# Performance work log

Hardware: AMD Instinct MI355X
Metric: run time of the kernel (lower is better)

The kernel has to match this reference:

```python
import jax, jax.numpy as jnp
import numpy as np
from jax import lax

B, N, T, NX = 4, 512, 24, 8
H = 64
PRED_LEN, NY = 12, 1
E_RAND = 8192
EPS = 1e-5


def setup_inputs() -> dict:
    key = jax.random.key(0)
    ks = jax.random.split(key, 24)
    sc = lambda k, shape: (jax.random.normal(k, shape, jnp.float32) * 0.05)
    x = jax.random.normal(ks[0], (B, N, T, NX), jnp.float32)
    er = jax.random.randint(ks[1], (2, E_RAND), 0, N, dtype=jnp.int32)
    loops = jnp.stack([jnp.arange(N, dtype=jnp.int32), jnp.arange(N, dtype=jnp.int32)])
    edge_index = jnp.concatenate([er, loops], axis=1)  # [2, 8704]
    return {
        'x': x,
        'edge_index': edge_index,
        'W_fc': sc(ks[2], (NX, H)), 'b_fc': jnp.zeros((H,), jnp.float32),
        'W1': sc(ks[3], (H, H)), 'a_l1': sc(ks[4], (H,)), 'a_r1': sc(ks[5], (H,)), 'bias1': jnp.zeros((H,), jnp.float32),
        'W2': sc(ks[6], (H, H)), 'a_l2': sc(ks[7], (H,)), 'a_r2': sc(ks[8], (H,)), 'bias2': jnp.zeros((H,), jnp.float32),
        'W_ih': sc(ks[9], (4 * H, H)), 'W_hh': sc(ks[10], (4 * H, H)),
        'b_ih': jnp.zeros((4 * H,), jnp.float32), 'b_hh': jnp.zeros((4 * H,), jnp.float32),
        'g_l': jnp.ones((H,), jnp.float32), 'b_l': jnp.zeros((H,), jnp.float32),
        'g_g': jnp.ones((H,), jnp.float32), 'b_g': jnp.zeros((H,), jnp.float32),
        'W_d': sc(ks[11], (H, PRED_LEN * NY)), 'b_d': jnp.zeros((PRED_LEN * NY,), jnp.float32),
    }


def _layer_norm(x, g, b):
    mu = jnp.mean(x, axis=-1, keepdims=True)
    var = jnp.mean(jnp.square(x - mu), axis=-1, keepdims=True)
    return (x - mu) * lax.rsqrt(var + EPS) * g + b


def _gat(x, W, a_l, a_r, bias, mask):
    # x: [B,N,T,F] -> operate in [B,T,N,H] layout (torch transpose(1,2))
    h = jnp.einsum('bntf,fh->btnh', x, W)          # [B,T,N,H]
    el = jnp.einsum('btnh,h->btn', h, a_l)          # attn_l
    er = jnp.einsum('btnh,h->btn', h, a_r)          # attn_r
    e = el[..., :, None] + er[..., None, :]         # [B,T,N,N]
    e = jax.nn.leaky_relu(e, negative_slope=0.2)
    e = jnp.where(mask, e, -jnp.inf)
    alpha = jax.nn.softmax(e, axis=-1)
    out = jnp.einsum('btmn,btnh->bmth', alpha, h) + bias  # back to [B,N,T,H]
    return jax.nn.gelu(out, approximate=False)


def _lstm(xseq, W_ih, W_hh, b_ih, b_hh):
    # xseq: [M, T, H] -> outputs [M, T, H]; PyTorch gate order i,f,g,o
    M = xseq.shape[0]
    Hh = W_hh.shape[1]
    b = b_ih + b_hh
    def step(carry, xt):
        hprev, cprev = carry
        gates = xt @ W_ih.T + hprev @ W_hh.T + b
        i, f, g, o = jnp.split(gates, 4, axis=-1)
        c = jax.nn.sigmoid(f) * cprev + jax.nn.sigmoid(i) * jnp.tanh(g)
        h = jax.nn.sigmoid(o) * jnp.tanh(c)
        return (h, c), h
    init = (jnp.zeros((M, Hh), xseq.dtype), jnp.zeros((M, Hh), xseq.dtype))
    _, hs = lax.scan(step, init, xseq.transpose(1, 0, 2))  # [T,M,H]
    return hs.transpose(1, 0, 2)


def reference(x, edge_index, W_fc, b_fc, W1, a_l1, a_r1, bias1, W2, a_l2, a_r2, bias2,
              W_ih, W_hh, b_ih, b_hh, g_l, b_l, g_g, b_g, W_d, b_d):
    Bb, Nn, Tt, _ = x.shape
    mask = jnp.zeros((Nn, Nn), bool).at[edge_index[0], edge_index[1]].set(True)
    x_h = jnp.einsum('bntf,fh->bnth', x, W_fc) + b_fc          # fc
    g1 = _gat(x_h, W1, a_l1, a_r1, bias1, mask)                # conv1
    g2 = _gat(g1, W2, a_l2, a_r2, bias2, mask)                 # conv2
    l = _lstm(x_h.reshape(Bb * Nn, Tt, -1), W_ih, W_hh, b_ih, b_hh).reshape(Bb, Nn, Tt, -1)
    h = _layer_norm(g2, g_g, b_g) + _layer_norm(l, g_l, b_l)
    last = h[:, :, -1, :]                                       # [B,N,H]
    out = last @ W_d + b_d                                      # [B,N,pred_len*ny]
    return out.reshape(Bb, Nn, PRED_LEN, NY)
```

## Files before the change

### kernel.cpp

```cpp
#include <hip/hip_runtime.h>
#include <hip/hip_bf16.h>
#include <math.h>

#define BB 4
#define NN 512
#define TT 24
#define NXF 8
#define HH 64
#define PRED 12
#define MM (BB*NN)

typedef __attribute__((ext_vector_type(8))) short short8;
typedef __attribute__((ext_vector_type(4))) float f32x4;

#define WS_HBUF    0
#define WS_H2      131072
#define WS_G2      262144
#define WS_EL      393216
#define WS_ER      395264
#define WS_EL2     397312
#define WS_ER2     399360
#define WS_WCOMB   401408
#define WS_BCOMB   403456
#define WS_WHHFRAG 403712

__device__ inline float sigm(float x){ return 1.f/(1.f+__expf(-x)); }
__device__ inline float tanh_fast(float x){ float e=__expf(2.f*x); return 1.f - 2.f/(e+1.f); }
__device__ inline float gelu_exact(float x){ return 0.5f*x*(1.f+erff(x*0.70710678118654752440f)); }
__device__ inline unsigned short f2bu(float f){
    unsigned b=__float_as_uint(f);
    return (unsigned short)((b + 0x7FFFu + ((b>>16)&1u))>>16);
}
__device__ inline float bu2f(unsigned short u){ return __uint_as_float(((unsigned)u)<<16); }

__device__ inline void split8(const float* f, short8& hi, short8& lo){
    #pragma unroll
    for (int j = 0; j < 8; ++j){
        unsigned short h = f2bu(f[j]);
        hi[j] = (short)h;
        lo[j] = (short)f2bu(f[j] - bu2f(h));
    }
}

__global__ __launch_bounds__(256,2) void gat1pre_kernel(
    const float* __restrict__ x, const float* __restrict__ Wfc, const float* __restrict__ bfc,
    const float* __restrict__ W1, const float* __restrict__ al1, const float* __restrict__ ar1,
    const float* __restrict__ Wih, const float* __restrict__ Whh,
    const float* __restrict__ bih, const float* __restrict__ bhh,
    float* __restrict__ Hbuf, float* __restrict__ el, float* __restrict__ er,
    float* __restrict__ wcombG, float* __restrict__ bcombG,
    unsigned short* __restrict__ whhfrag)
{
    __shared__ float sw1[HH*HH];
    __shared__ float swfc[NXF*HH];
    __shared__ float sb[HH], sal[HH], sar[HH];
    __shared__ float sxh[4][68];
    __shared__ float sx[4][NXF];
    const int t = threadIdx.x;

    if (blockIdx.x >= 512){
        const int f = blockIdx.x - 512;
        const int ng = t;
        float accf = 0.f, accb = 0.f;
        const float* wr = Wih + ng*64;
        #pragma unroll
        for (int k = 0; k < 64; ++k){
            float wv = wr[k];
            accf += Wfc[f*64 + k] * wv;
            accb += bfc[k] * wv;
        }
        wcombG[f*256 + ng] = accf;
        if (f == 0) bcombG[ng] = accb + bih[ng] + bhh[ng];
        #pragma unroll
        for (int u = 0; u < 8; ++u){
            int o = f*2048 + u*256 + t;
            int F  = o >> 9;
            int ln = (o >> 3) & 63;
            int j  = o & 7;
            int w_ = F >> 3, tt = (F >> 1) & 3, ks = F & 1;
            int q = ln >> 4, c = ln & 15;
            int ngx = (w_ + 4*tt)*16 + c;
            whhfrag[o] = f2bu(Whh[ngx*64 + ks*32 + q*8 + j]);
        }
        return;
    }

    const int r = t >> 6, h = t & 63;
    #pragma unroll
    for (int i = 0; i < 16; ++i) sw1[t + 256*i] = W1[t + 256*i];
    swfc[t] = Wfc[t];
    swfc[t+256] = Wfc[t+256];
    if (t < 64) sb[t] = bfc[t];
    else if (t < 128) sal[t-64] = al1[t-64];
    else if (t < 192) sar[t-128] = ar1[t-128];
    if (t < 32){
        int rr = t >> 3, f = t & 7;
        sx[rr][f] = x[(size_t)(blockIdx.x*4 + rr)*(TT*NXF) + (TT-1)*NXF + f];
    }
    __syncthreads();
    float xh = sb[h];
    #pragma unroll
    for (int f = 0; f < NXF; ++f) xh += sx[r][f]*swfc[f*HH + h];
    sxh[r][h] = xh;
    __syncthreads();
    float acc = 0.f;
    const float4* xr = (const float4*)&sxh[r][0];
    #pragma unroll
    for (int k4 = 0; k4 < 16; ++k4){
        float4 xv = xr[k4];
        acc += xv.x*sw1[(4*k4+0)*HH+h] + xv.y*sw1[(4*k4+1)*HH+h]
             + xv.z*sw1[(4*k4+2)*HH+h] + xv.w*sw1[(4*k4+3)*HH+h];
    }
    const int m = blockIdx.x*4 + r;
    Hbuf[(size_t)m*HH + h] = acc;
    float v1 = acc*sal[h], v2 = acc*sar[h];
    #pragma unroll
    for (int o = 32; o; o >>= 1){ v1 += __shfl_xor(v1,o); v2 += __shfl_xor(v2,o); }
    if (h == 0){ el[m] = v1; er[m] = v2; }
}

__global__ __launch_bounds__(256,2) void attn_fuse_kernel(
    const float* __restrict__ Hbuf, const float* __restrict__ el_in, const float* __restrict__ er_in,
    const int* __restrict__ ei, int E,
    const float* __restrict__ bias1,
    const float* __restrict__ W2, const float* __restrict__ al2, const float* __restrict__ ar2,
    float* __restrict__ H2, float* __restrict__ el2, float* __restrict__ er2)
{
    __shared__ unsigned smask[16][16];
    __shared__ float er_s[NN];
    __shared__ float alpha[16][516];
    __shared__ __align__(16) float uSpace[64*70];
    __shared__ float xh2[16][68];
    __shared__ float sal[HH], sar[HH];

    const int t = threadIdx.x;
    const int b = blockIdx.x >> 5;
    const int m0 = (blockIdx.x & 31) * 16;
    const int l = t & 63, w = t >> 6;
    const int quad = l >> 4, c16 = l & 15;
    float (*HT)[70] = (float(*)[70])uSpace;

    if (t < 64) sal[t] = al2[t]; else if (t < 128) sar[t-64] = ar2[t-64];
    ((unsigned*)smask)[t] = 0;
    er_s[t] = er_in[b*NN + t];
    er_s[t+256] = er_in[b*NN + t + 256];
    __syncthreads();
    for (int e = t; e < E; e += 256){
        int s = ei[e];
        unsigned rl = (unsigned)(s - m0);
        if (rl < 16u){
            int d = ei[E + e];
            atomicOr(&smask[rl][d>>5], 1u << (d & 31));
        }
    }
    const float* Hbase = Hbuf + (size_t)b*NN*HH;
    const int nn = t >> 2, cc = t & 3;
    float4 r0,r1,r2,r3;
    {
        const float4* src = (const float4*)(Hbase + (size_t)nn*HH + cc*16);
        r0 = src[0]; r1 = src[1]; r2 = src[2]; r3 = src[3];
    }
    __syncthreads();
    for (int q = 0; q < 4; ++q){
        const int i = w*4 + q;
        const float elv = el_in[b*NN + m0 + i];
        float e8[8]; unsigned mk = 0; float mx = -1e30f;
        #pragma unroll
        for (int j = 0; j < 8; ++j){
            int n = l + 64*j;
            float ev = elv + er_s[n];
            ev = ev >= 0.f ? ev : 0.2f*ev;
            unsigned mb = (smask[i][(l>>5) + 2*j] >> (l & 31)) & 1u;
            e8[j] = ev;
            if (mb){ mk |= (1u<<j); mx = fmaxf(mx, ev); }
        }
        #pragma unroll
        for (int o = 32; o; o >>= 1) mx = fmaxf(mx, __shfl_xor(mx, o));
        float s = 0.f;
        #pragma unroll
        for (int j = 0; j < 8; ++j){
            float p = ((mk>>j) & 1u) ? __expf(e8[j]-mx) : 0.f;
            e8[j] = p; s += p;
        }
        #pragma unroll
        for (int o = 32; o; o >>= 1) s += __shfl_xor(s, o);
        const float inv = 1.f/s;
        #pragma unroll
        for (int j = 0; j < 8; ++j) alpha[i][l + 64*j] = e8[j]*inv;
    }
    __syncthreads();

    f32x4 acc = {0.f,0.f,0.f,0.f};
    for (int tile = 0; tile < 8; ++tile){
        {
            float v[16] = {r0.x,r0.y,r0.z,r0.w, r1.x,r1.y,r1.z,r1.w,
                           r2.x,r2.y,r2.z,r2.w, r3.x,r3.y,r3.z,r3.w};
            #pragma unroll
            for (int jj = 0; jj < 16; ++jj) HT[cc*16 + jj][nn] = v[jj];
        }
        if (tile < 7){
            const float4* src = (const float4*)(Hbase + (size_t)((tile+1)*64 + nn)*HH + cc*16);
            r0 = src[0]; r1 = src[1]; r2 = src[2]; r3 = src[3];
        }
        __syncthreads();
        #pragma unroll
        for (int ks = 0; ks < 2; ++ks){
            const int k0 = tile*64 + ks*32;
            const float* ap = &alpha[c16][k0 + quad*8];
            float4 a0 = *(const float4*)ap;
            float4 a1 = *(const float4*)(ap + 4);
            const float* bp = &HT[w*16 + c16][ks*32 + quad*8];
            float2 b0 = *(const float2*)bp,     b1 = *(const float2*)(bp+2);
            float2 b2 = *(const float2*)(bp+4), b3 = *(const float2*)(bp+6);
            float af[8] = {a0.x,a0.y,a0.z,a0.w,a1.x,a1.y,a1.z,a1.w};
            float bf[8] = {b0.x,b0.y,b1.x,b1.y,b2.x,b2.y,b3.x,b3.y};
            short8 ahi, alo, bhi, blo;
            split8(af, ahi, alo);
            split8(bf, bhi, blo);
            acc = __builtin_amdgcn_mfma_f32_16x16x32_bf16(ahi, bhi, acc, 0,0,0);
            acc = __builtin_amdgcn_mfma_f32_16x16x32_bf16(alo, bhi, acc, 0,0,0);
            acc = __builtin_amdgcn_mfma_f32_16x16x32_bf16(ahi, blo, acc, 0,0,0);
        }
        __syncthreads();
    }
    {
        const int h = w*16 + c16;
        const float bv = bias1[h];
        #pragma unroll
        for (int reg = 0; reg < 4; ++reg)
            xh2[quad*4 + reg][h] = gelu_exact(acc[reg] + bv);
    }
    __syncthreads();
    float* sw2 = uSpace;
    #pragma unroll
    for (int i = 0; i < 16; ++i) sw2[t + 256*i] = W2[t + 256*i];
    __syncthreads();
    {
        const int h = l;
        for (int q = 0; q < 4; ++q){
            const int i = w + 4*q;
            float acc2 = 0.f;
            const float4* xr = (const float4*)&xh2[i][0];
            #pragma unroll
            for (int k4 = 0; k4 < 16; ++k4){
                float4 xv = xr[k4];
                acc2 += xv.x*sw2[(4*k4+0)*HH+h] + xv.y*sw2[(4*k4+1)*HH+h]
                      + xv.z*sw2[(4*k4+2)*HH+h] + xv.w*sw2[(4*k4+3)*HH+h];
            }
            const int m = b*NN + m0 + i;
            H2[(size_t)m*HH + h] = acc2;
            float v1 = acc2*sal[h], v2 = acc2*sar[h];
            #pragma unroll
            for (int o = 32; o; o >>= 1){ v1 += __shfl_xor(v1,o); v2 += __shfl_xor(v2,o); }
            if (h == 0){ el2[m] = v1; er2[m] = v2; }
        }
    }
}

__global__ __launch_bounds__(256,2) void attn2_kernel(
    const float* __restrict__ Hbuf, const float* __restrict__ el_in, const float* __restrict__ er_in,
    const int* __restrict__ ei, int E,
    const float* __restrict__ bias2, float* __restrict__ g2)
{
    __shared__ unsigned smask[16][16];
    __shared__ float er_s[NN];
    __shared__ float alpha[16][516];
    __shared__ __align__(16) float uSpace[64*70];
    const int t = threadIdx.x;
    const int b = blockIdx.x >> 5;
    const int m0 = (blockIdx.x & 31) * 16;
    const int l = t & 63, w = t >> 6;
    const int quad = l >> 4, c16 = l & 15;
    float (*HT)[70] = (float(*)[70])uSpace;

    ((unsigned*)smask)[t] = 0;
    er_s[t] = er_in[b*NN + t];
    er_s[t+256] = er_in[b*NN + t + 256];
    __syncthreads();
    for (int e = t; e < E; e += 256){
        int s = ei[e];
        unsigned rl = (unsigned)(s - m0);
        if (rl < 16u){
            int d = ei[E + e];
            atomicOr(&smask[rl][d>>5], 1u << (d & 31));
        }
    }
    const float* Hbase = Hbuf + (size_t)b*NN*HH;
    const int nn = t >> 2, cc = t & 3;
    float4 r0,r1,r2,r3;
    {
        const float4* src = (const float4*)(Hbase + (size_t)nn*HH + cc*16);
        r0 = src[0]; r1 = src[1]; r2 = src[2]; r3 = src[3];
    }
    __syncthreads();
    for (int q = 0; q < 4; ++q){
        const int i = w*4 + q;
        const float elv = el_in[b*NN + m0 + i];
        float e8[8]; unsigned mk = 0; float mx = -1e30f;
        #pragma unroll
        for (int j = 0; j < 8; ++j){
            int n = l + 64*j;
            float ev = elv + er_s[n];
            ev = ev >= 0.f ? ev : 0.2f*ev;
            unsigned mb = (smask[i][(l>>5) + 2*j] >> (l & 31)) & 1u;
            e8[j] = ev;
            if (mb){ mk |= (1u<<j); mx = fmaxf(mx, ev); }
        }
        #pragma unroll
        for (int o = 32; o; o >>= 1) mx = fmaxf(mx, __shfl_xor(mx, o));
        float s = 0.f;
        #pragma unroll
        for (int j = 0; j < 8; ++j){
            float p = ((mk>>j) & 1u) ? __expf(e8[j]-mx) : 0.f;
            e8[j] = p; s += p;
        }
        #pragma unroll
        for (int o = 32; o; o >>= 1) s += __shfl_xor(s, o);
        const float inv = 1.f/s;
        #pragma unroll
        for (int j = 0; j < 8; ++j) alpha[i][l + 64*j] = e8[j]*inv;
    }
    __syncthreads();

    f32x4 acc = {0.f,0.f,0.f,0.f};
    for (int tile = 0; tile < 8; ++tile){
        {
            float v[16] = {r0.x,r0.y,r0.z,r0.w, r1.x,r1.y,r1.z,r1.w,
                           r2.x,r2.y,r2.z,r2.w, r3.x,r3.y,r3.z,r3.w};
            #pragma unroll
            for (int jj = 0; jj < 16; ++jj) HT[cc*16 + jj][nn] = v[jj];
        }
        if (tile < 7){
            const float4* src = (const float4*)(Hbase + (size_t)((tile+1)*64 + nn)*HH + cc*16);
            r0 = src[0]; r1 = src[1]; r2 = src[2]; r3 = src[3];
        }
        __syncthreads();
        #pragma unroll
        for (int ks = 0; ks < 2; ++ks){
            const int k0 = tile*64 + ks*32;
            const float* ap = &alpha[c16][k0 + quad*8];
            float4 a0 = *(const float4*)ap;
            float4 a1 = *(const float4*)(ap + 4);
            const float* bp = &HT[w*16 + c16][ks*32 + quad*8];
            float2 b0 = *(const float2*)bp,     b1 = *(const float2*)(bp+2);
            float2 b2 = *(const float2*)(bp+4), b3 = *(const float2*)(bp+6);
            float af[8] = {a0.x,a0.y,a0.z,a0.w,a1.x,a1.y,a1.z,a1.w};
            float bf[8] = {b0.x,b0.y,b1.x,b1.y,b2.x,b2.y,b3.x,b3.y};
            short8 ahi, alo, bhi, blo;
            split8(af, ahi, alo);
            split8(bf, bhi, blo);
            acc = __builtin_amdgcn_mfma_f32_16x16x32_bf16(ahi, bhi, acc, 0,0,0);
            acc = __builtin_amdgcn_mfma_f32_16x16x32_bf16(alo, bhi, acc, 0,0,0);
            acc = __builtin_amdgcn_mfma_f32_16x16x32_bf16(ahi, blo, acc, 0,0,0);
        }
        __syncthreads();
    }
    {
        const int h = w*16 + c16;
        const float bv = bias2[h];
        #pragma unroll
        for (int reg = 0; reg < 4; ++reg)
            g2[(size_t)(b*NN + m0 + quad*4 + reg)*HH + h] = gelu_exact(acc[reg] + bv);
    }
}

#define LHS 72
#define LXS 40
__global__ __launch_bounds__(256,2) void lstm_final_kernel(
    const float* __restrict__ x,
    const float* __restrict__ wcombG, const float* __restrict__ bcombG,
    const unsigned short* __restrict__ whhfrag,
    const float* __restrict__ g2,
    const float* __restrict__ g_l, const float* __restrict__ b_l,
    const float* __restrict__ g_g, const float* __restrict__ b_g,
    const float* __restrict__ W_d, const float* __restrict__ b_d,
    float* __restrict__ out)
{
    __shared__ __align__(16) unsigned short hbi[2][16*LHS];
    __shared__ __align__(16) unsigned short hlo[2][16*LHS];
    __shared__ __align__(16) unsigned short xls[TT*16*LXS];
    __shared__ float hfin[16*HH];

    const int t = threadIdx.x;
    const int m0 = blockIdx.x * 16;
    const int lane = t & 63;
    const int w = t >> 6;
    const int quad = lane >> 4;
    const int c16 = lane & 15;

    {
        unsigned* h0 = (unsigned*)hbi[0];
        unsigned* l0 = (unsigned*)hlo[0];
        for (int i = t; i < 16*LHS/2; i += 256){ h0[i] = 0u; l0[i] = 0u; }
        unsigned* xw = (unsigned*)xls;
        for (int i = t; i < TT*16*LXS/2; i += 256) xw[i] = 0u;
    }
    short8 bw[4][2]; short8 bx[4]; float bc[4];
    #pragma unroll
    for (int tt = 0; tt < 4; ++tt){
        const int ng = (w + 4*tt)*16 + c16;
        bc[tt] = bcombG[ng];
        #pragma unroll
        for (int ks = 0; ks < 2; ++ks)
            bw[tt][ks] = *(const short8*)&whhfrag[(((w*4+tt)*2)+ks)*512 + lane*8];
        short8 vx = {0,0,0,0,0,0,0,0};
        if (quad == 0){
            #pragma unroll
            for (int j = 0; j < 8; ++j) vx[j] = (short)f2bu(wcombG[j*256 + ng]);
        }
        bx[tt] = vx;
    }
    __syncthreads();
    for (int i = t; i < 16*TT*NXF; i += 256){
        int r = i / (TT*NXF);
        int rem = i - r*(TT*NXF);
        int st = rem >> 3, f = rem & 7;
        xls[st*(16*LXS) + r*LXS + f] = f2bu(x[(size_t)(m0+r)*(TT*NXF) + rem]);
    }
    __syncthreads();

    float cst[4] = {0,0,0,0};
    float hf[4]  = {0,0,0,0};

    for (int st = 0; st < TT; ++st){
        const int p = st & 1;
        const unsigned short* hb = hbi[p];
        const unsigned short* hl_ = hlo[p];
        short8 ahi0 = *(const short8*)&hb[c16*LHS + quad*8];
        short8 ahi1 = *(const short8*)&hb[c16*LHS + 32 + quad*8];
        short8 alo0 = *(const short8*)&hl_[c16*LHS + quad*8];
        short8 alo1 = *(const short8*)&hl_[c16*LHS + 32 + quad*8];
        short8 ax   = *(const short8*)&xls[st*(16*LXS) + c16*LXS + quad*8];
        f32x4 acc[4];
        #pragma unroll
        for (int tt = 0; tt < 4; ++tt){
            f32x4 a = {bc[tt], bc[tt], bc[tt], bc[tt]};
            a = __builtin_amdgcn_mfma_f32_16x16x32_bf16(ax,   bx[tt],    a, 0,0,0);
            a = __builtin_amdgcn_mfma_f32_16x16x32_bf16(ahi0, bw[tt][0], a, 0,0,0);
            a = __builtin_amdgcn_mfma_f32_16x16x32_bf16(ahi1, bw[tt][1], a, 0,0,0);
            a = __builtin_amdgcn_mfma_f32_16x16x32_bf16(alo0, bw[tt][0], a, 0,0,0);
            a = __builtin_amdgcn_mfma_f32_16x16x32_bf16(alo1, bw[tt][1], a, 0,0,0);
            acc[tt] = a;
        }
        unsigned short* ho = hbi[p^1];
        unsigned short* lo_o = hlo[p^1];
        #pragma unroll
        for (int reg = 0; reg < 4; ++reg){
            float gi = acc[0][reg], gf = acc[1][reg], gg = acc[2][reg], go = acc[3][reg];
            float cn = sigm(gf)*cst[reg] + sigm(gi)*tanh_fast(gg);
            cst[reg] = cn;
            float hn = sigm(go)*tanh_fast(cn);
            hf[reg] = hn;
            unsigned short hu = f2bu(hn);
            float lov = hn - bu2f(hu);
            int addr = (quad*4+reg)*LHS + w*16 + c16;
            ho[addr] = hu;
            lo_o[addr] = f2bu(lov);
        }
        __syncthreads();
    }

    #pragma unroll
    for (int reg = 0; reg < 4; ++reg)
        hfin[(quad*4+reg)*HH + w*16 + c16] = hf[reg];
    __syncthreads();
    float* sdec = (float*)xls;
    const int h = lane;
    for (int q = 0; q < 4; ++q){
        const int ml = w*4 + q;
        float lv = hfin[ml*HH + h];
        float gv = g2[(size_t)(m0+ml)*HH + h];

        float s1 = gv;
        #pragma unroll
        for (int o = 32; o; o >>= 1) s1 += __shfl_xor(s1, o);
        float dg = gv - s1*(1.f/64.f);
        float v1 = dg*dg;
        #pragma unroll
        for (int o = 32; o; o >>= 1) v1 += __shfl_xor(v1, o);
        float lng = dg*rsqrtf(v1*(1.f/64.f) + 1e-5f)*g_g[h] + b_g[h];

        float s2 = lv;
        #pragma unroll
        for (int o = 32; o; o >>= 1) s2 += __shfl_xor(s2, o);
        float dl = lv - s2*(1.f/64.f);
        float v2 = dl*dl;
        #pragma unroll
        for (int o = 32; o; o >>= 1) v2 += __shfl_xor(v2, o);
        float lnl = dl*rsqrtf(v2*(1.f/64.f) + 1e-5f)*g_l[h] + b_l[h];

        sdec[ml*HH + h] = lng + lnl;
    }
    __syncthreads();
    if (t < 16*PRED){
        int rr = t / PRED, pp = t - rr*PRED;
        float acc = b_d[pp];
        #pragma unroll
        for (int k = 0; k < HH; ++k) acc += sdec[rr*HH + k]*W_d[k*PRED + pp];
        out[(size_t)(m0+rr)*PRED + pp] = acc;
    }
}

extern "C" void kernel_launch(void* const* d_in, const int* in_sizes, int n_in,
                              void* d_out, int out_size, void* d_ws, size_t ws_size,
                              hipStream_t stream){
    const float* x    = (const float*)d_in[0];
    const int*   ei   = (const int*)  d_in[1];
    const float* Wfc  = (const float*)d_in[2];
    const float* bfc  = (const float*)d_in[3];
    const float* W1   = (const float*)d_in[4];
    const float* al1  = (const float*)d_in[5];
    const float* ar1  = (const float*)d_in[6];
    const float* bias1= (const float*)d_in[7];
    const float* W2   = (const float*)d_in[8];
    const float* al2  = (const float*)d_in[9];
    const float* ar2  = (const float*)d_in[10];
    const float* bias2= (const float*)d_in[11];
    const float* Wih  = (const float*)d_in[12];
    const float* Whh  = (const float*)d_in[13];
    const float* bih  = (const float*)d_in[14];
    const float* bhh  = (const float*)d_in[15];
    const float* g_l  = (const float*)d_in[16];
    const float* b_l  = (const float*)d_in[17];
    const float* g_g  = (const float*)d_in[18];
    const float* b_g  = (const float*)d_in[19];
    const float* W_d  = (const float*)d_in[20];
    const float* b_d  = (const float*)d_in[21];

    float* ws = (float*)d_ws;
    const int E = in_sizes[1] / 2;

    gat1pre_kernel<<<512 + 8, 256, 0, stream>>>(x, Wfc, bfc, W1, al1, ar1,
                                                Wih, Whh, bih, bhh,
                                                ws+WS_HBUF, ws+WS_EL, ws+WS_ER,
                                                ws+WS_WCOMB, ws+WS_BCOMB,
                                                (unsigned short*)(ws+WS_WHHFRAG));
    attn_fuse_kernel<<<BB*(NN/16), 256, 0, stream>>>(ws+WS_HBUF, ws+WS_EL, ws+WS_ER,
                                                     ei, E, bias1, W2, al2, ar2,
                                                     ws+WS_H2, ws+WS_EL2, ws+WS_ER2);
    attn2_kernel<<<BB*(NN/16), 256, 0, stream>>>(ws+WS_H2, ws+WS_EL2, ws+WS_ER2,
                                                 ei, E, bias2, ws+WS_G2);
    lstm_final_kernel<<<MM/16, 256, 0, stream>>>(x, ws+WS_WCOMB, ws+WS_BCOMB,
                                                 (const unsigned short*)(ws+WS_WHHFRAG),
                                                 ws+WS_G2, g_l, b_l, g_g, b_g, W_d, b_d,
                                                 (float*)d_out);
}
```

Measured before the change: 180.5 us.

## Run LSTM alongside GAT layer-1 attention and fuse layernorm/decoder into attn2

The LSTM recurrence moves into the same launch as the first attention kernel, in extra blocks (128 attention blocks plus 128 LSTM blocks), so the two independent stages run concurrently instead of back to back. The layernorm and decoder epilogue moves into the second attention kernel, which keeps g2 in shared memory instead of writing it to global memory. This drops one launch and one global round trip for g2. In exchange the LSTM hidden state goes through the workspace, shared memory is a single manually carved buffer, and the LSTM blocks now serially gate the mid kernel, so the 24-step recurrence sits on the critical path alongside attention.

```diff
diff --git a/kernel.cpp b/kernel.cpp
--- a/kernel.cpp
+++ b/kernel.cpp
@@ -12,10 +12,11 @@
 
 typedef __attribute__((ext_vector_type(8))) short short8;
 typedef __attribute__((ext_vector_type(4))) float f32x4;
+typedef unsigned short ushort;
 
 #define WS_HBUF    0
 #define WS_H2      131072
-#define WS_G2      262144
+#define WS_HL      262144
 #define WS_EL      393216
 #define WS_ER      395264
 #define WS_EL2     397312
@@ -27,16 +28,16 @@
 __device__ inline float sigm(float x){ return 1.f/(1.f+__expf(-x)); }
 __device__ inline float tanh_fast(float x){ float e=__expf(2.f*x); return 1.f - 2.f/(e+1.f); }
 __device__ inline float gelu_exact(float x){ return 0.5f*x*(1.f+erff(x*0.70710678118654752440f)); }
-__device__ inline unsigned short f2bu(float f){
+__device__ inline ushort f2bu(float f){
     unsigned b=__float_as_uint(f);
-    return (unsigned short)((b + 0x7FFFu + ((b>>16)&1u))>>16);
+    return (ushort)((b + 0x7FFFu + ((b>>16)&1u))>>16);
 }
-__device__ inline float bu2f(unsigned short u){ return __uint_as_float(((unsigned)u)<<16); }
+__device__ inline float bu2f(ushort u){ return __uint_as_float(((unsigned)u)<<16); }
 
 __device__ inline void split8(const float* f, short8& hi, short8& lo){
     #pragma unroll
     for (int j = 0; j < 8; ++j){
-        unsigned short h = f2bu(f[j]);
+        ushort h = f2bu(f[j]);
         hi[j] = (short)h;
         lo[j] = (short)f2bu(f[j] - bu2f(h));
     }
@@ -49,7 +50,7 @@
     const float* __restrict__ bih, const float* __restrict__ bhh,
     float* __restrict__ Hbuf, float* __restrict__ el, float* __restrict__ er,
     float* __restrict__ wcombG, float* __restrict__ bcombG,
-    unsigned short* __restrict__ whhfrag)
+    ushort* __restrict__ whhfrag)
 {
     __shared__ float sw1[HH*HH];
     __shared__ float swfc[NXF*HH];
@@ -119,25 +120,120 @@
     if (h == 0){ el[m] = v1; er[m] = v2; }
 }
 
-__global__ __launch_bounds__(256,2) void attn_fuse_kernel(
+#define LHS 72
+#define LXS 40
+__global__ __launch_bounds__(256,2) void mid_fused_kernel(
     const float* __restrict__ Hbuf, const float* __restrict__ el_in, const float* __restrict__ er_in,
     const int* __restrict__ ei, int E,
     const float* __restrict__ bias1,
     const float* __restrict__ W2, const float* __restrict__ al2, const float* __restrict__ ar2,
-    float* __restrict__ H2, float* __restrict__ el2, float* __restrict__ er2)
+    float* __restrict__ H2, float* __restrict__ el2, float* __restrict__ er2,
+    const float* __restrict__ x,
+    const float* __restrict__ wcombG, const float* __restrict__ bcombG,
+    const ushort* __restrict__ whhfrag,
+    float* __restrict__ hl)
 {
-    __shared__ unsigned smask[16][16];
-    __shared__ float er_s[NN];
-    __shared__ float alpha[16][516];
-    __shared__ __align__(16) float uSpace[64*70];
-    __shared__ float xh2[16][68];
-    __shared__ float sal[HH], sar[HH];
-
+    __shared__ __align__(16) char smem[58880];
     const int t = threadIdx.x;
+    const int lane = t & 63;
+    const int w = t >> 6;
+    const int quad = lane >> 4;
+    const int c16 = lane & 15;
+
+    if (blockIdx.x >= 128){
+        ushort* hbi = (ushort*)smem;
+        ushort* hlo = (ushort*)(smem + 4608);
+        ushort* xls = (ushort*)(smem + 9216);
+        const int m0 = (blockIdx.x - 128) * 16;
+
+        {
+            unsigned* h0 = (unsigned*)hbi;
+            unsigned* l0 = (unsigned*)hlo;
+            for (int i = t; i < 2*16*LHS/2; i += 256){ h0[i] = 0u; l0[i] = 0u; }
+            unsigned* xw = (unsigned*)xls;
+            for (int i = t; i < TT*16*LXS/2; i += 256) xw[i] = 0u;
+        }
+        short8 bw[4][2]; short8 bx[4]; float bc[4];
+        #pragma unroll
+        for (int tt = 0; tt < 4; ++tt){
+            const int ng = (w + 4*tt)*16 + c16;
+            bc[tt] = bcombG[ng];
+            #pragma unroll
+            for (int ks = 0; ks < 2; ++ks)
+                bw[tt][ks] = *(const short8*)&whhfrag[(((w*4+tt)*2)+ks)*512 + lane*8];
+            short8 vx = {0,0,0,0,0,0,0,0};
+            if (quad == 0){
+                #pragma unroll
+                for (int j = 0; j < 8; ++j) vx[j] = (short)f2bu(wcombG[j*256 + ng]);
+            }
+            bx[tt] = vx;
+        }
+        __syncthreads();
+        for (int i = t; i < 16*TT*NXF; i += 256){
+            int r = i / (TT*NXF);
+            int rem = i - r*(TT*NXF);
+            int st = rem >> 3, f = rem & 7;
+            xls[st*(16*LXS) + r*LXS + f] = f2bu(x[(size_t)(m0+r)*(TT*NXF) + rem]);
+        }
+        __syncthreads();
+
+        float cst[4] = {0,0,0,0};
+        float hf[4]  = {0,0,0,0};
+
+        for (int st = 0; st < TT; ++st){
+            const int p = st & 1;
+            const ushort* hb  = hbi + p*(16*LHS);
+            const ushort* hl_ = hlo + p*(16*LHS);
+            short8 ahi0 = *(const short8*)&hb[c16*LHS + quad*8];
+            short8 ahi1 = *(const short8*)&hb[c16*LHS + 32 + quad*8];
+            short8 alo0 = *(const short8*)&hl_[c16*LHS + quad*8];
+            short8 alo1 = *(const short8*)&hl_[c16*LHS + 32 + quad*8];
+            short8 ax   = *(const short8*)&xls[st*(16*LXS) + c16*LXS + quad*8];
+            f32x4 acc[4];
+            #pragma unroll
+            for (int tt = 0; tt < 4; ++tt){
+                f32x4 a = {bc[tt], bc[tt], bc[tt], bc[tt]};
+                a = __builtin_amdgcn_mfma_f32_16x16x32_bf16(ax,   bx[tt],    a, 0,0,0);
+                a = __builtin_amdgcn_mfma_f32_16x16x32_bf16(ahi0, bw[tt][0], a, 0,0,0);
+                a = __builtin_amdgcn_mfma_f32_16x16x32_bf16(ahi1, bw[tt][1], a, 0,0,0);
+                a = __builtin_amdgcn_mfma_f32_16x16x32_bf16(alo0, bw[tt][0], a, 0,0,0);
+                a = __builtin_amdgcn_mfma_f32_16x16x32_bf16(alo1, bw[tt][1], a, 0,0,0);
+                acc[tt] = a;
+            }
+            ushort* ho   = hbi + (p^1)*(16*LHS);
+            ushort* lo_o = hlo + (p^1)*(16*LHS);
+            #pragma unroll
+            for (int reg = 0; reg < 4; ++reg){
+                float gi = acc[0][reg], gf = acc[1][reg], gg = acc[2][reg], go = acc[3][reg];
+                float cn = sigm(gf)*cst[reg] + sigm(gi)*tanh_fast(gg);
+                cst[reg] = cn;
+                float hn = sigm(go)*tanh_fast(cn);
+                hf[reg] = hn;
+                ushort hu = f2bu(hn);
+                float lov = hn - bu2f(hu);
+                int addr = (quad*4+reg)*LHS + w*16 + c16;
+                ho[addr] = hu;
+                lo_o[addr] = f2bu(lov);
+            }
+            __syncthreads();
+        }
+        #pragma unroll
+        for (int reg = 0; reg < 4; ++reg)
+            hl[(size_t)(m0 + quad*4 + reg)*HH + w*16 + c16] = hf[reg];
+        return;
+    }
+
+    unsigned (*smask)[16] = (unsigned(*)[16])smem;
+    float* er_s  = (float*)(smem + 1024);
+    float* sal   = (float*)(smem + 3072);
+    float* sar   = (float*)(smem + 3328);
+    float (*alpha)[516] = (float(*)[516])(smem + 3584);
+    float* uSpace = (float*)(smem + 36608);
+    float (*xh2)[68] = (float(*)[68])(smem + 54528);
+
     const int b = blockIdx.x >> 5;
     const int m0 = (blockIdx.x & 31) * 16;
-    const int l = t & 63, w = t >> 6;
-    const int quad = l >> 4, c16 = l & 15;
+    const int l = lane;
     float (*HT)[70] = (float(*)[70])uSpace;
 
     if (t < 64) sal[t] = al2[t]; else if (t < 128) sar[t-64] = ar2[t-64];
@@ -257,15 +353,22 @@
     }
 }
 
-__global__ __launch_bounds__(256,2) void attn2_kernel(
+__global__ __launch_bounds__(256,2) void attn2_final_kernel(
     const float* __restrict__ Hbuf, const float* __restrict__ el_in, const float* __restrict__ er_in,
     const int* __restrict__ ei, int E,
-    const float* __restrict__ bias2, float* __restrict__ g2)
+    const float* __restrict__ bias2,
+    const float* __restrict__ hl,
+    const float* __restrict__ g_l, const float* __restrict__ b_l,
+    const float* __restrict__ g_g, const float* __restrict__ b_g,
+    const float* __restrict__ W_d, const float* __restrict__ b_d,
+    float* __restrict__ out)
 {
-    __shared__ unsigned smask[16][16];
-    __shared__ float er_s[NN];
-    __shared__ float alpha[16][516];
-    __shared__ __align__(16) float uSpace[64*70];
+    __shared__ __align__(16) char smem[54016];
+    unsigned (*smask)[16] = (unsigned(*)[16])smem;
+    float* er_s  = (float*)(smem + 1024);
+    float (*alpha)[516] = (float(*)[516])(smem + 3072);
+    float* uSpace = (float*)(smem + 36096);
+
     const int t = threadIdx.x;
     const int b = blockIdx.x >> 5;
     const int m0 = (blockIdx.x & 31) * 16;
@@ -355,149 +458,52 @@
         }
         __syncthreads();
     }
+    float* sg2  = (float*)(smem + 3072);
+    float* sdec = (float*)(smem + 36096);
     {
         const int h = w*16 + c16;
         const float bv = bias2[h];
         #pragma unroll
         for (int reg = 0; reg < 4; ++reg)
-            g2[(size_t)(b*NN + m0 + quad*4 + reg)*HH + h] = gelu_exact(acc[reg] + bv);
-    }
-}
-
-#define LHS 72
-#define LXS 40
-__global__ __launch_bounds__(256,2) void lstm_final_kernel(
-    const float* __restrict__ x,
-    const float* __restrict__ wcombG, const float* __restrict__ bcombG,
-    const unsigned short* __restrict__ whhfrag,
-    const float* __restrict__ g2,
-    const float* __restrict__ g_l, const float* __restrict__ b_l,
-    const float* __restrict__ g_g, const float* __restrict__ b_g,
-    const float* __restrict__ W_d, const float* __restrict__ b_d,
-    float* __restrict__ out)
-{
-    __shared__ __align__(16) unsigned short hbi[2][16*LHS];
-    __shared__ __align__(16) unsigned short hlo[2][16*LHS];
-    __shared__ __align__(16) unsigned short xls[TT*16*LXS];
-    __shared__ float hfin[16*HH];
-
-    const int t = threadIdx.x;
-    const int m0 = blockIdx.x * 16;
-    const int lane = t & 63;
-    const int w = t >> 6;
-    const int quad = lane >> 4;
-    const int c16 = lane & 15;
-
+            sg2[(quad*4 + reg)*HH + h] = gelu_exact(acc[reg] + bv);
+    }
+    __syncthreads();
+    const int gbase = b*NN + m0;
     {
-        unsigned* h0 = (unsigned*)hbi[0];
-        unsigned* l0 = (unsigned*)hlo[0];
-        for (int i = t; i < 16*LHS/2; i += 256){ h0[i] = 0u; l0[i] = 0u; }
-        unsigned* xw = (unsigned*)xls;
-        for (int i = t; i < TT*16*LXS/2; i += 256) xw[i] = 0u;
-    }
-    short8 bw[4][2]; short8 bx[4]; float bc[4];
-    #pragma unroll
-    for (int tt = 0; tt < 4; ++tt){
-        const int ng = (w + 4*tt)*16 + c16;
-        bc[tt] = bcombG[ng];
-        #pragma unroll
-        for (int ks = 0; ks < 2; ++ks)
-            bw[tt][ks] = *(const short8*)&whhfrag[(((w*4+tt)*2)+ks)*512 + lane*8];
-        short8 vx = {0,0,0,0,0,0,0,0};
-        if (quad == 0){
-            #pragma unroll
-            for (int j = 0; j < 8; ++j) vx[j] = (short)f2bu(wcombG[j*256 + ng]);
-        }
-        bx[tt] = vx;
-    }
-    __syncthreads();
-    for (int i = t; i < 16*TT*NXF; i += 256){
-        int r = i / (TT*NXF);
-        int rem = i - r*(TT*NXF);
-        int st = rem >> 3, f = rem & 7;
-        xls[st*(16*LXS) + r*LXS + f] = f2bu(x[(size_t)(m0+r)*(TT*NXF) + rem]);
-    }
-    __syncthreads();
-
-    float cst[4] = {0,0,0,0};
-    float hf[4]  = {0,0,0,0};
-
-    for (int st = 0; st < TT; ++st){
-        const int p = st & 1;
-        const unsigned short* hb = hbi[p];
-        const unsigned short* hl_ = hlo[p];
-        short8 ahi0 = *(const short8*)&hb[c16*LHS + quad*8];
-        short8 ahi1 = *(const short8*)&hb[c16*LHS + 32 + quad*8];
-        short8 alo0 = *(const short8*)&hl_[c16*LHS + quad*8];
-        short8 alo1 = *(const short8*)&hl_[c16*LHS + 32 + quad*8];
-        short8 ax   = *(const short8*)&xls[st*(16*LXS) + c16*LXS + quad*8];
-        f32x4 acc[4];
-        #pragma unroll
-        for (int tt = 0; tt < 4; ++tt){
-            f32x4 a = {bc[tt], bc[tt], bc[tt], bc[tt]};
-            a = __builtin_amdgcn_mfma_f32_16x16x32_bf16(ax,   bx[tt],    a, 0,0,0);
-            a = __builtin_amdgcn_mfma_f32_16x16x32_bf16(ahi0, bw[tt][0], a, 0,0,0);
-            a = __builtin_amdgcn_mfma_f32_16x16x32_bf16(ahi1, bw[tt][1], a, 0,0,0);
-            a = __builtin_amdgcn_mfma_f32_16x16x32_bf16(alo0, bw[tt][0], a, 0,0,0);
-            a = __builtin_amdgcn_mfma_f32_16x16x32_bf16(alo1, bw[tt][1], a, 0,0,0);
-            acc[tt] = a;
-        }
-        unsigned short* ho = hbi[p^1];
-        unsigned short* lo_o = hlo[p^1];
-        #pragma unroll
-        for (int reg = 0; reg < 4; ++reg){
-            float gi = acc[0][reg], gf = acc[1][reg], gg = acc[2][reg], go = acc[3][reg];
-            float cn = sigm(gf)*cst[reg] + sigm(gi)*tanh_fast(gg);
-            cst[reg] = cn;
-            float hn = sigm(go)*tanh_fast(cn);
-            hf[reg] = hn;
-            unsigned short hu = f2bu(hn);
-            float lov = hn - bu2f(hu);
-            int addr = (quad*4+reg)*LHS + w*16 + c16;
-            ho[addr] = hu;
-            lo_o[addr] = f2bu(lov);
-        }
-        __syncthreads();
-    }
-
-    #pragma unroll
-    for (int reg = 0; reg < 4; ++reg)
-        hfin[(quad*4+reg)*HH + w*16 + c16] = hf[reg];
-    __syncthreads();
-    float* sdec = (float*)xls;
-    const int h = lane;
-    for (int q = 0; q < 4; ++q){
-        const int ml = w*4 + q;
-        float lv = hfin[ml*HH + h];
-        float gv = g2[(size_t)(m0+ml)*HH + h];
-
-        float s1 = gv;
-        #pragma unroll
-        for (int o = 32; o; o >>= 1) s1 += __shfl_xor(s1, o);
-        float dg = gv - s1*(1.f/64.f);
-        float v1 = dg*dg;
-        #pragma unroll
-        for (int o = 32; o; o >>= 1) v1 += __shfl_xor(v1, o);
-        float lng = dg*rsqrtf(v1*(1.f/64.f) + 1e-5f)*g_g[h] + b_g[h];
-
-        float s2 = lv;
-        #pragma unroll
-        for (int o = 32; o; o >>= 1) s2 += __shfl_xor(s2, o);
-        float dl = lv - s2*(1.f/64.f);
-        float v2 = dl*dl;
-        #pragma unroll
-        for (int o = 32; o; o >>= 1) v2 += __shfl_xor(v2, o);
-        float lnl = dl*rsqrtf(v2*(1.f/64.f) + 1e-5f)*g_l[h] + b_l[h];
-
-        sdec[ml*HH + h] = lng + lnl;
+        const int h = l;
+        for (int q = 0; q < 4; ++q){
+            const int ml = w*4 + q;
+            float gv = sg2[ml*HH + h];
+            float lv = hl[(size_t)(gbase + ml)*HH + h];
+
+            float s1 = gv;
+            #pragma unroll
+            for (int o = 32; o; o >>= 1) s1 += __shfl_xor(s1, o);
+            float dg = gv - s1*(1.f/64.f);
+            float v1 = dg*dg;
+            #pragma unroll
+            for (int o = 32; o; o >>= 1) v1 += __shfl_xor(v1, o);
+            float lng = dg*rsqrtf(v1*(1.f/64.f) + 1e-5f)*g_g[h] + b_g[h];
+
+            float s2 = lv;
+            #pragma unroll
+            for (int o = 32; o; o >>= 1) s2 += __shfl_xor(s2, o);
+            float dl = lv - s2*(1.f/64.f);
+            float v2 = dl*dl;
+            #pragma unroll
+            for (int o = 32; o; o >>= 1) v2 += __shfl_xor(v2, o);
+            float lnl = dl*rsqrtf(v2*(1.f/64.f) + 1e-5f)*g_l[h] + b_l[h];
+
+            sdec[ml*HH + h] = lng + lnl;
+        }
     }
     __syncthreads();
     if (t < 16*PRED){
         int rr = t / PRED, pp = t - rr*PRED;
-        float acc = b_d[pp];
-        #pragma unroll
-        for (int k = 0; k < HH; ++k) acc += sdec[rr*HH + k]*W_d[k*PRED + pp];
-        out[(size_t)(m0+rr)*PRED + pp] = acc;
+        float a = b_d[pp];
+        #pragma unroll
+        for (int k = 0; k < HH; ++k) a += sdec[rr*HH + k]*W_d[k*PRED + pp];
+        out[(size_t)(gbase + rr)*PRED + pp] = a;
     }
 }
 
@@ -534,14 +540,16 @@
                                                 Wih, Whh, bih, bhh,
                                                 ws+WS_HBUF, ws+WS_EL, ws+WS_ER,
                                                 ws+WS_WCOMB, ws+WS_BCOMB,
-                                                (unsigned short*)(ws+WS_WHHFRAG));
-    attn_fuse_kernel<<<BB*(NN/16), 256, 0, stream>>>(ws+WS_HBUF, ws+WS_EL, ws+WS_ER,
-                                                     ei, E, bias1, W2, al2, ar2,
-                                                     ws+WS_H2, ws+WS_EL2, ws+WS_ER2);
-    attn2_kernel<<<BB*(NN/16), 256, 0, stream>>>(ws+WS_H2, ws+WS_EL2, ws+WS_ER2,
-                                                 ei, E, bias2, ws+WS_G2);
-    lstm_final_kernel<<<MM/16, 256, 0, stream>>>(x, ws+WS_WCOMB, ws+WS_BCOMB,
-                                                 (const unsigned short*)(ws+WS_WHHFRAG),
-                                                 ws+WS_G2, g_l, b_l, g_g, b_g, W_d, b_d,
-                                                 (float*)d_out);
+                                                (ushort*)(ws+WS_WHHFRAG));
+    mid_fused_kernel<<<256, 256, 0, stream>>>(ws+WS_HBUF, ws+WS_EL, ws+WS_ER,
+                                              ei, E, bias1, W2, al2, ar2,
+                                              ws+WS_H2, ws+WS_EL2, ws+WS_ER2,
+                                              x, ws+WS_WCOMB, ws+WS_BCOMB,
+                                              (const ushort*)(ws+WS_WHHFRAG),
+                                              ws+WS_HL);
+    attn2_final_kernel<<<BB*(NN/16), 256, 0, stream>>>(ws+WS_H2, ws+WS_EL2, ws+WS_ER2,
+                                                       ei, E, bias2,
+                                                       ws+WS_HL,
+                                                       g_l, b_l, g_g, b_g, W_d, b_d,
+                                                       (float*)d_out);
 }
```

New measurement: 150.7 us. 16.5% less time.
